# Kernel tuning notes

Measured on AMD Instinct MI355X. Metric: run time of the kernel, lower is better.

Reference implementation:

```python
import jax, jax.numpy as jnp
from jax import lax
import numpy as np

# Quantization / layer config (mirrors QuantizedConv2d init_kwargs)
IN_ZP = 3
OUT_ZP = -2
IN_SCALE = 0.05
OUT_SCALE = 0.1
STRIDE = (1, 1)
PAD = (1, 1)  # (pad_h, pad_w)
DILATION = (1, 1)
GROUPS = 1
FEATURE_BITS = 8
Q_MIN, Q_MAX = -(1 << (FEATURE_BITS - 1)), (1 << (FEATURE_BITS - 1)) - 1  # -128, 127


def setup_inputs() -> dict:
    key = jax.random.key(0)
    k1, k2, k3, k4 = jax.random.split(key, 4)
    N, Cin, H, W = 32, 128, 56, 56
    Cout, KH, KW = 256, 3, 3
    x = jax.random.randint(k1, (N, Cin, H, W), -128, 128, dtype=jnp.int8)
    weight = jax.random.randint(k2, (Cout, Cin, KH, KW), -128, 128, dtype=jnp.int8)
    bias = jax.random.randint(k3, (Cout,), -1000, 1000, dtype=jnp.int32)  # shifted quantized bias
    weight_scale = jax.random.uniform(k4, (Cout,), dtype=jnp.float32, minval=1e-3, maxval=1e-2)
    return {"x": x, "weight": weight, "bias": bias, "weight_scale": weight_scale}


def reference(x, weight, bias, weight_scale):
    # q_y = round((CONV[q_x, q_w] + shifted_bias) * (S_x * S_w / S_y) + Z_y), clamped to int8
    # Pad with the input zero point (NOT zero), matching F.pad(..., value=input_zero_point)
    ph, pw = PAD
    xp = jnp.pad(x, ((0, 0), (0, 0), (ph, ph), (pw, pw)), constant_values=IN_ZP)
    # Exact integer convolution (matches the CPU int32 path; GPU float path rounds
    # back to the same int32 values)
    acc = lax.conv_general_dilated(
        xp.astype(jnp.int32), weight.astype(jnp.int32),
        window_strides=STRIDE, padding='VALID',
        rhs_dilation=DILATION, feature_group_count=GROUPS,
        dimension_numbers=('NCHW', 'OIHW', 'NCHW'))  # [N, Cout, H, W] int32
    acc = acc + bias[None, :, None, None]
    # Fused dequant/requant epilogue: per-channel scale, output zero point, round, clamp
    scale = (IN_SCALE * weight_scale / OUT_SCALE)[None, :, None, None]  # [1, Cout, 1, 1]
    y = acc.astype(jnp.float32) * scale + jnp.float32(OUT_ZP)
    return jnp.clip(jnp.round(y), Q_MIN, Q_MAX).astype(jnp.int8)
```

## Files before the change

### kernel.cpp

```cpp
#include <hip/hip_runtime.h>


#define NB    32
#define CIN   128
#define HH    56
#define WW    56
#define COUT  256
#define HP    58
#define WP    58
#define PIX   (HH*WW)
#define KTOT  1152
#define NCHUNK 18

#define NPT   28
#define BN    112
#define NJ    7
#define PHB1  (NJ*1024)
#define PL    (HP*WP*64)
#define BPB   (2*PL)

typedef int v4i __attribute__((ext_vector_type(4)));

#define GLOAD_LDS(gsrc, ldst) \
    __builtin_amdgcn_global_load_lds( \
        (const __attribute__((address_space(1))) void*)(gsrc), \
        (__attribute__((address_space(3))) void*)(ldst), 16, 0, 0)

__global__ void pack_both_kernel(const int* __restrict__ x,
                                 unsigned char* __restrict__ xp8,
                                 const int* __restrict__ wt,
                                 unsigned char* __restrict__ w8f,
                                 int n0) {
    __shared__ unsigned int lt[WW * 33];
    int bx = blockIdx.x;
    int tid = threadIdx.x;

    if (bx < COUT) {
        int co = bx;
        for (int idx = tid; idx < KTOT/4; idx += 256) {
            int k  = idx * 4;
            int r  = k >> 7;
            int ci = k & 127;
            const int* wb = wt + ((co*CIN + ci)*9 + r);
            int v0 = wb[0], v1 = wb[9], v2 = wb[18], v3 = wb[27];
            unsigned int pack = (v0 & 0xFF) | ((v1 & 0xFF) << 8) |
                                ((v2 & 0xFF) << 16) | ((unsigned)(v3 & 0xFF) << 24);
            int tch = k >> 6;
            size_t dst = ((size_t)((tch*16 + (co >> 4))*16 + (co & 15)))*64 + (k & 63);
            *(unsigned int*)(w8f + dst) = pack;
        }
        return;
    }

    int bxx = bx - COUT;
    int nl = bxx / HP;
    int hp = bxx % HP;
    int nb = n0 + nl;
    unsigned char* slab = xp8 + (size_t)nl * BPB;
    unsigned int* q0 = (unsigned int*)(slab + (size_t)hp * WP * 64);
    unsigned int* q1 = (unsigned int*)(slab + PL + (size_t)hp * WP * 64);

    if (hp == 0 || hp == HP-1) {
        const v4i zp = {0x03030303, 0x03030303, 0x03030303, 0x03030303};
        v4i* a0 = (v4i*)q0;
        v4i* a1 = (v4i*)q1;
        for (int i = tid; i < (WP*64)/16; i += 256) { a0[i] = zp; a1[i] = zp; }
        return;
    }

    int h  = hp - 1;
    int wl = tid & 63;
    int cg = tid >> 6;
    if (wl < WW) {
        const int s = HH*WW;
#pragma unroll
        for (int k = 0; k < 8; ++k) {
            int ci0 = cg*4 + k*16;
            const int* xb = x + (((size_t)(nb*CIN + ci0)*HH + h)*WW + wl);
            int v0 = xb[0], v1 = xb[s], v2 = xb[2*s], v3 = xb[3*s];
            unsigned int pack = (v0 & 0xFF) | ((v1 & 0xFF) << 8) |
                                ((v2 & 0xFF) << 16) | ((unsigned)(v3 & 0xFF) << 24);
            lt[wl*33 + (ci0 >> 2)] = pack;
        }
    }
    __syncthreads();

#pragma unroll
    for (int it = 0; it < 7; ++it) {
        int idx = it*256 + tid;
        int p = idx >> 5;
        int d = idx & 31;
        unsigned int* qq = (d < 16) ? q0 : q1;
        qq[(p + 1)*16 + (d & 15)] = lt[p*33 + d];
    }
    if (tid < 64) {
        int d = tid & 15;
        unsigned int* qq = (tid & 16) ? q1 : q0;
        int col = (tid & 32) ? (WP-1) : 0;
        qq[col*16 + d] = 0x03030303u;
    }
}

__device__ __forceinline__ int koff_of(int t) {
    int r  = t >> 1;
    int kh = (r >= 6) ? 2 : (r >= 3 ? 1 : 0);
    int kw = r - kh*3;
    return (t & 1) * PL + ((kh*WP + kw) << 6);
}

__launch_bounds__(512, 4)
__global__ void conv_kernel(const unsigned char* __restrict__ w8f,
                            const unsigned char* __restrict__ xp8,
                            const int* __restrict__ bias,
                            const float* __restrict__ wscale,
                            int* __restrict__ out,
                            int n0) {
    __shared__ __align__(16) unsigned char ldsB[3*PHB1];

    int nwg = gridDim.x;
    int bx0 = blockIdx.x;
    int q = nwg >> 3, r = nwg & 7;
    int xcd = bx0 & 7, idx8 = bx0 >> 3;
    int bx = (xcd < r ? xcd*(q+1) : r*(q+1) + (xcd-r)*q) + idx8;

    int pt = bx % NPT;
    int nl = bx / NPT;
    int nb = n0 + nl;
    int p0 = pt * BN;

    int tid  = threadIdx.x;
    int lane = tid & 63;
    int wm   = tid >> 6;
    int lr   = lane & 15;
    int lg   = lane >> 4;

    int l4 = lane >> 2;
    int sw = (lane & 3) ^ ((lane >> 3) & 3);
    int slot = (wm < 7) ? wm : 6;
    int slotu = __builtin_amdgcn_readfirstlane(slot);
    int pS = p0 + slot*16 + l4;
    int ph = pS / WW, pw = pS % WW;
    const unsigned char* bsrc =
        xp8 + (size_t)nl*BPB + ((size_t)(ph*WP + pw))*64 + sw*16;

    int rslot = lg ^ ((lr >> 1) & 3);
    int vb = lr*64 + rslot*16;

    const unsigned char* abase =
        w8f + (size_t)(wm*2)*1024 + (lr*64 + lg*16);

    v4i acc[2][NJ];
#pragma unroll
    for (int i = 0; i < 2; ++i)
#pragma unroll
        for (int j = 0; j < NJ; ++j)
            acc[i][j] = (v4i){0, 0, 0, 0};

#define STAGE1(T) \
    GLOAD_LDS(bsrc + koff_of(T), &ldsB[((T)%3)*PHB1 + slotu*1024])

    STAGE1(0);

#pragma unroll
    for (int p = 0; p < NCHUNK; ++p) {
        v4i a_[2];
#pragma unroll
        for (int i = 0; i < 2; ++i)
            a_[i] = *(const v4i*)(abase + (size_t)p*16384 + i*1024);
        __builtin_amdgcn_sched_barrier(0);
        if (p < NCHUNK-1) STAGE1(p+1);

        if (p < NCHUNK-1) asm volatile("s_waitcnt vmcnt(3)" ::: "memory");
        else              asm volatile("s_waitcnt vmcnt(2)" ::: "memory");
        __builtin_amdgcn_sched_barrier(0);
        __builtin_amdgcn_s_barrier();

        int roff = (p % 3) * PHB1;
        v4i b_[NJ];
#pragma unroll
        for (int j = 0; j < NJ; ++j)
            b_[j] = *(const v4i*)&ldsB[roff + vb + j*1024];
        __builtin_amdgcn_s_setprio(1);
#pragma unroll
        for (int i = 0; i < 2; ++i)
#pragma unroll
            for (int j = 0; j < NJ; ++j)
                acc[i][j] = __builtin_amdgcn_mfma_i32_16x16x64_i8(
                    a_[i], b_[j], acc[i][j], 0, 0, 0);
        __builtin_amdgcn_s_setprio(0);
    }
#undef STAGE1

#pragma unroll
    for (int i = 0; i < 2; ++i) {
#pragma unroll
        for (int rr = 0; rr < 4; ++rr) {
            int co = wm*32 + i*16 + lg*4 + rr;
            float sc = __fdiv_rn(__fmul_rn(0.05f, wscale[co]), 0.1f);
            int bs = bias[co];
            int* orow = out + ((size_t)(nb*COUT + co))*PIX + p0;
#pragma unroll
            for (int j = 0; j < NJ; ++j) {
                float accf = (float)(acc[i][j][rr] + bs);
                float y = __fadd_rn(__fmul_rn(accf, sc), -2.0f);
                y = rintf(y);
                y = fminf(fmaxf(y, -128.0f), 127.0f);
                orow[j*16 + lr] = (int)y;
            }
        }
    }
}

__launch_bounds__(256)
__global__ void conv_direct_kernel(const int* __restrict__ x,
                                   const int* __restrict__ wt,
                                   const int* __restrict__ bias,
                                   const float* __restrict__ wscale,
                                   int* __restrict__ out) {
    size_t idx = (size_t)blockIdx.x * 256 + threadIdx.x;
    if (idx >= (size_t)NB * COUT * PIX) return;
    int w  = idx % WW;
    int h  = (idx / WW) % HH;
    int co = (idx / PIX) % COUT;
    int nb = idx / ((size_t)PIX * COUT);
    int acc = 0;
    for (int ci = 0; ci < CIN; ++ci) {
        const int* xb = x + ((size_t)(nb*CIN + ci)*HH)*WW;
        const int* wb = wt + ((size_t)(co*CIN + ci)*9);
        for (int kh = 0; kh < 3; ++kh) {
            int hh = h + kh - 1;
            for (int kw = 0; kw < 3; ++kw) {
                int ww2 = w + kw - 1;
                int xv = (hh >= 0 && hh < HH && ww2 >= 0 && ww2 < WW)
                         ? xb[hh*WW + ww2] : 3;
                acc += xv * wb[kh*3 + kw];
            }
        }
    }
    float sc = __fdiv_rn(__fmul_rn(0.05f, wscale[co]), 0.1f);
    float y = __fadd_rn(__fmul_rn((float)(acc + bias[co]), sc), -2.0f);
    y = rintf(y);
    y = fminf(fmaxf(y, -128.0f), 127.0f);
    out[idx] = (int)y;
}

extern "C" void kernel_launch(void* const* d_in, const int* in_sizes, int n_in,
                              void* d_out, int out_size, void* d_ws, size_t ws_size,
                              hipStream_t stream) {
    const int*   x      = (const int*)d_in[0];
    const int*   weight = (const int*)d_in[1];
    const int*   bias   = (const int*)d_in[2];
    const float* wscale = (const float*)d_in[3];
    int*         out    = (int*)d_out;

    const size_t XOFF = 320u << 10;
    const size_t SLAB = (size_t)COUT * PIX * 4;

    size_t navail = (ws_size > XOFF) ? (ws_size - XOFF) / BPB : 0;

    unsigned char* w8f = (unsigned char*)d_ws;
    unsigned char* xpw = (unsigned char*)d_ws + XOFF;

    if (navail >= 4) {
        int wsN = (int)(navail < 32 ? navail : 32);
        int Na  = 32 - wsN;
        unsigned char* xpt = (unsigned char*)d_out + (size_t)Na * SLAB;

        if (Na > 0) {
            pack_both_kernel<<<dim3(COUT + Na*HP), dim3(256), 0, stream>>>(
                x, xpt, weight, w8f, 0);
            pack_both_kernel<<<dim3(COUT + wsN*HP), dim3(256), 0, stream>>>(
                x, xpw, weight, w8f, Na);
            conv_kernel<<<dim3(NPT*Na), dim3(512), 0, stream>>>(
                w8f, xpt, bias, wscale, out, 0);
            conv_kernel<<<dim3(NPT*wsN), dim3(512), 0, stream>>>(
                w8f, xpw, bias, wscale, out, Na);
        } else {
            pack_both_kernel<<<dim3(COUT + 32*HP), dim3(256), 0, stream>>>(
                x, xpw, weight, w8f, 0);
            conv_kernel<<<dim3(NPT*32), dim3(512), 0, stream>>>(
                w8f, xpw, bias, wscale, out, 0);
        }
    } else if (navail >= 1) {
        int nchk = navail >= 2 ? 2 : 1;
        for (int n0 = 0; n0 < NB; n0 += nchk) {
            int nc = (NB - n0 < nchk) ? (NB - n0) : nchk;
            pack_both_kernel<<<dim3(COUT + nc*HP), dim3(256), 0, stream>>>(
                x, xpw, weight, w8f, n0);
            conv_kernel<<<dim3(NPT*nc), dim3(512), 0, stream>>>(
                w8f, xpw, bias, wscale, out, n0);
        }
    } else {
        size_t total = (size_t)NB * COUT * PIX;
        conv_direct_kernel<<<dim3((total + 255) / 256), dim3(256), 0, stream>>>(
            x, weight, bias, wscale, out);
    }
}
```

Before: 58.10 us.

## Retile conv into 128-pixel by 128-channel blocks with 4-stage LDS pipeline

```diff
diff --git a/kernel.cpp b/kernel.cpp
--- a/kernel.cpp
+++ b/kernel.cpp
@@ -12,10 +12,9 @@
 #define KTOT  1152
 #define NCHUNK 18
 
-#define NPT   28
-#define BN    112
-#define NJ    7
-#define PHB1  (NJ*1024)
+#define NTP   25
+#define BNP   128
+#define CHBY  (BNP*64)
 #define PL    (HP*WP*64)
 #define BPB   (2*PL)
 
@@ -108,14 +107,14 @@
     return (t & 1) * PL + ((kh*WP + kw) << 6);
 }
 
-__launch_bounds__(512, 4)
+__launch_bounds__(256, 4)
 __global__ void conv_kernel(const unsigned char* __restrict__ w8f,
                             const unsigned char* __restrict__ xp8,
                             const int* __restrict__ bias,
                             const float* __restrict__ wscale,
                             int* __restrict__ out,
                             int n0) {
-    __shared__ __align__(16) unsigned char ldsB[3*PHB1];
+    __shared__ __align__(16) unsigned char ldsB[4*CHBY];
 
     int nwg = gridDim.x;
     int bx0 = blockIdx.x;
@@ -123,89 +122,105 @@
     int xcd = bx0 & 7, idx8 = bx0 >> 3;
     int bx = (xcd < r ? xcd*(q+1) : r*(q+1) + (xcd-r)*q) + idx8;
 
-    int pt = bx % NPT;
-    int nl = bx / NPT;
+    int ch = bx & 1;
+    int rest = bx >> 1;
+    int pt = rest % NTP;
+    int nl = rest / NTP;
     int nb = n0 + nl;
-    int p0 = pt * BN;
+    int p0 = pt * BNP;
 
     int tid  = threadIdx.x;
     int lane = tid & 63;
     int wm   = tid >> 6;
+    int pxg  = wm >> 1;
+    int cosub = wm & 1;
     int lr   = lane & 15;
     int lg   = lane >> 4;
 
     int l4 = lane >> 2;
     int sw = (lane & 3) ^ ((lane >> 3) & 3);
-    int slot = (wm < 7) ? wm : 6;
-    int slotu = __builtin_amdgcn_readfirstlane(slot);
-    int pS = p0 + slot*16 + l4;
-    int ph = pS / WW, pw = pS % WW;
-    const unsigned char* bsrc =
-        xp8 + (size_t)nl*BPB + ((size_t)(ph*WP + pw))*64 + sw*16;
+    int s0u = __builtin_amdgcn_readfirstlane(wm*2);
+    int s1u = __builtin_amdgcn_readfirstlane(wm*2+1);
+    int pS0 = p0 + (wm*2)*16 + l4;
+    int pS1 = p0 + (wm*2+1)*16 + l4;
+    if (pS0 >= PIX) pS0 = PIX-1;
+    if (pS1 >= PIX) pS1 = PIX-1;
+    const unsigned char* bsrc0 =
+        xp8 + (size_t)nl*BPB + ((size_t)((pS0/WW)*WP + pS0%WW))*64 + sw*16;
+    const unsigned char* bsrc1 =
+        xp8 + (size_t)nl*BPB + ((size_t)((pS1/WW)*WP + pS1%WW))*64 + sw*16;
 
     int rslot = lg ^ ((lr >> 1) & 3);
-    int vb = lr*64 + rslot*16;
+    int vb = pxg*4096 + lr*64 + rslot*16;
 
     const unsigned char* abase =
-        w8f + (size_t)(wm*2)*1024 + (lr*64 + lg*16);
-
-    v4i acc[2][NJ];
-#pragma unroll
-    for (int i = 0; i < 2; ++i)
-#pragma unroll
-        for (int j = 0; j < NJ; ++j)
+        w8f + (size_t)(ch*8 + cosub*4)*1024 + (lr*64 + lg*16);
+
+    v4i acc[4][4];
+#pragma unroll
+    for (int i = 0; i < 4; ++i)
+#pragma unroll
+        for (int j = 0; j < 4; ++j)
             acc[i][j] = (v4i){0, 0, 0, 0};
 
-#define STAGE1(T) \
-    GLOAD_LDS(bsrc + koff_of(T), &ldsB[((T)%3)*PHB1 + slotu*1024])
-
-    STAGE1(0);
+#define STAGE2(T) do {                                                         \
+        int k_ = koff_of(T);                                                   \
+        GLOAD_LDS(bsrc0 + k_, &ldsB[((T)&3)*CHBY + s0u*1024]);                 \
+        GLOAD_LDS(bsrc1 + k_, &ldsB[((T)&3)*CHBY + s1u*1024]);                 \
+    } while (0)
+
+    STAGE2(0);
+    STAGE2(1);
 
 #pragma unroll
     for (int p = 0; p < NCHUNK; ++p) {
-        v4i a_[2];
-#pragma unroll
-        for (int i = 0; i < 2; ++i)
+        v4i a_[4];
+#pragma unroll
+        for (int i = 0; i < 4; ++i)
             a_[i] = *(const v4i*)(abase + (size_t)p*16384 + i*1024);
         __builtin_amdgcn_sched_barrier(0);
-        if (p < NCHUNK-1) STAGE1(p+1);
-
-        if (p < NCHUNK-1) asm volatile("s_waitcnt vmcnt(3)" ::: "memory");
-        else              asm volatile("s_waitcnt vmcnt(2)" ::: "memory");
+        if (p < NCHUNK-2) STAGE2(p+2);
+
+        if (p == 0)             asm volatile("s_waitcnt vmcnt(8)"  ::: "memory");
+        else if (p < NCHUNK-2)  asm volatile("s_waitcnt vmcnt(12)" ::: "memory");
+        else if (p == NCHUNK-2) asm volatile("s_waitcnt vmcnt(10)" ::: "memory");
+        else                    asm volatile("s_waitcnt vmcnt(8)"  ::: "memory");
         __builtin_amdgcn_sched_barrier(0);
         __builtin_amdgcn_s_barrier();
 
-        int roff = (p % 3) * PHB1;
-        v4i b_[NJ];
-#pragma unroll
-        for (int j = 0; j < NJ; ++j)
+        int roff = (p & 3) * CHBY;
+        v4i b_[4];
+#pragma unroll
+        for (int j = 0; j < 4; ++j)
             b_[j] = *(const v4i*)&ldsB[roff + vb + j*1024];
         __builtin_amdgcn_s_setprio(1);
 #pragma unroll
-        for (int i = 0; i < 2; ++i)
-#pragma unroll
-            for (int j = 0; j < NJ; ++j)
+        for (int i = 0; i < 4; ++i)
+#pragma unroll
+            for (int j = 0; j < 4; ++j)
                 acc[i][j] = __builtin_amdgcn_mfma_i32_16x16x64_i8(
                     a_[i], b_[j], acc[i][j], 0, 0, 0);
         __builtin_amdgcn_s_setprio(0);
     }
-#undef STAGE1
-
-#pragma unroll
-    for (int i = 0; i < 2; ++i) {
+#undef STAGE2
+
+    int px0 = p0 + pxg*64;
+#pragma unroll
+    for (int i = 0; i < 4; ++i) {
 #pragma unroll
         for (int rr = 0; rr < 4; ++rr) {
-            int co = wm*32 + i*16 + lg*4 + rr;
+            int co = ch*128 + cosub*64 + i*16 + lg*4 + rr;
             float sc = __fdiv_rn(__fmul_rn(0.05f, wscale[co]), 0.1f);
             int bs = bias[co];
-            int* orow = out + ((size_t)(nb*COUT + co))*PIX + p0;
-#pragma unroll
-            for (int j = 0; j < NJ; ++j) {
+            int* orow = out + ((size_t)(nb*COUT + co))*PIX + px0;
+#pragma unroll
+            for (int j = 0; j < 4; ++j) {
+                int px = px0 + j*16 + lr;
                 float accf = (float)(acc[i][j][rr] + bs);
                 float y = __fadd_rn(__fmul_rn(accf, sc), -2.0f);
                 y = rintf(y);
                 y = fminf(fmaxf(y, -128.0f), 127.0f);
-                orow[j*16 + lr] = (int)y;
+                if (px < PIX) orow[j*16 + lr] = (int)y;
             }
         }
     }
@@ -271,14 +286,14 @@
                 x, xpt, weight, w8f, 0);
             pack_both_kernel<<<dim3(COUT + wsN*HP), dim3(256), 0, stream>>>(
                 x, xpw, weight, w8f, Na);
-            conv_kernel<<<dim3(NPT*Na), dim3(512), 0, stream>>>(
+            conv_kernel<<<dim3(2*NTP*Na), dim3(256), 0, stream>>>(
                 w8f, xpt, bias, wscale, out, 0);
-            conv_kernel<<<dim3(NPT*wsN), dim3(512), 0, stream>>>(
+            conv_kernel<<<dim3(2*NTP*wsN), dim3(256), 0, stream>>>(
                 w8f, xpw, bias, wscale, out, Na);
         } else {
             pack_both_kernel<<<dim3(COUT + 32*HP), dim3(256), 0, stream>>>(
                 x, xpw, weight, w8f, 0);
-            conv_kernel<<<dim3(NPT*32), dim3(512), 0, stream>>>(
+            conv_kernel<<<dim3(2*NTP*32), dim3(256), 0, stream>>>(
                 w8f, xpw, bias, wscale, out, 0);
         }
     } else if (navail >= 1) {
@@ -287,7 +302,7 @@
             int nc = (NB - n0 < nchk) ? (NB - n0) : nchk;
             pack_both_kernel<<<dim3(COUT + nc*HP), dim3(256), 0, stream>>>(
                 x, xpw, weight, w8f, n0);
-            conv_kernel<<<dim3(NPT*nc), dim3(512), 0, stream>>>(
+            conv_kernel<<<dim3(2*NTP*nc), dim3(256), 0, stream>>>(
                 w8f, xpw, bias, wscale, out, n0);
         }
     } else {
```

New measurement: 77.61 us. +33.6%, slower.
